# Performance work log

Hardware: AMD Instinct MI355X
Metric: run time of the kernel (lower is better)

## Reference

```python
import jax, jax.numpy as jnp
import numpy as np

DIM = 512
NUM_HEADS = 8
HEAD_DIM = DIM // NUM_HEADS
SCALE = HEAD_DIM ** -0.5


def setup_inputs() -> dict:
    key = jax.random.key(0)
    k1, k2, k3, k4 = jax.random.split(key, 4)
    x = jax.random.normal(k1, (2, 4096, DIM), dtype=jnp.float32)
    # Linear weights stored as (in, out) for x @ W; torch Linear(dim, 3*dim, bias=False)
    w_qkv = jax.random.normal(k2, (DIM, 3 * DIM), dtype=jnp.float32) * (DIM ** -0.5)
    w_proj = jax.random.normal(k3, (DIM, DIM), dtype=jnp.float32) * (DIM ** -0.5)
    b_proj = jax.random.normal(k4, (DIM,), dtype=jnp.float32) * 0.02
    return {"x": x, "w_qkv": w_qkv, "w_proj": w_proj, "b_proj": b_proj}


def reference(x, w_qkv, w_proj, b_proj):
    B, N, C = x.shape
    qkv = (x @ w_qkv).reshape(B, N, 3, NUM_HEADS, HEAD_DIM)
    qkv = jnp.transpose(qkv, (2, 0, 3, 1, 4))  # (3, B, H, N, hd)
    q, k, v = qkv[0], qkv[1], qkv[2]
    attn = jnp.einsum("bhnd,bhmd->bhnm", q, k) * SCALE
    attn = jax.nn.softmax(attn, axis=-1)
    out = jnp.einsum("bhnm,bhmd->bhnd", attn, v)
    out = jnp.transpose(out, (0, 2, 1, 3)).reshape(B, N, C)
    return out @ w_proj + b_proj
```

## Files before the change

kernel.cpp:

```cpp
#include <hip/hip_runtime.h>
#include <hip/hip_bf16.h>
#include <stdint.h>
#include <math.h>

#define NC3 1536
#define QSCALE 0.18033688011111907f
#define KSPLIT 2

typedef __attribute__((ext_vector_type(8))) short short8;
typedef __attribute__((ext_vector_type(4))) short short4v;
typedef __attribute__((ext_vector_type(4))) float f32x4;
typedef __attribute__((ext_vector_type(16))) float f32x16;
typedef __attribute__((ext_vector_type(8))) _Float16 f16x8;
typedef __attribute__((ext_vector_type(2))) __fp16 fp16x2;

static __device__ __forceinline__ short f2bf(float f) {
    union { __hip_bfloat16 h; short s; } u;
    u.h = __float2bfloat16(f);
    return u.s;
}
static __device__ __forceinline__ float bf2f(short s) {
    return __uint_as_float(((unsigned)(unsigned short)s) << 16);
}
static __device__ __forceinline__ short f2h(float f) {
    union { __fp16 h; short s; } u;
    u.h = (__fp16)f;
    return u.s;
}
static __device__ __forceinline__ unsigned hpack(float a, float b) {
    union { fp16x2 h; unsigned u; } c;
    c.h = __builtin_amdgcn_cvt_pkrtz(a, b);
    return c.u;
}

#define GLD_LDS(g, l)                                                          \
    __builtin_amdgcn_global_load_lds(                                          \
        (const __attribute__((address_space(1))) void*)(g),                    \
        (__attribute__((address_space(3))) void*)(l), 16, 0, 0)

__global__ __launch_bounds__(256) void prep(const float* __restrict__ x,
                                            short* __restrict__ xbf,
                                            const float* __restrict__ wqkv,
                                            short* __restrict__ wqkvT,
                                            const float* __restrict__ wproj,
                                            short* __restrict__ wprojT) {
    int tx = threadIdx.x, ty = threadIdx.y;
    int tid = ty * 32 + tx;
    if (blockIdx.z == 0) {
        int bid = blockIdx.y * 48 + blockIdx.x;
        for (int i = bid * 256 + tid; i < 1048576; i += 768 * 256) {
            float4 v = ((const float4*)x)[i];
            short4v o = {f2bf(v.x), f2bf(v.y), f2bf(v.z), f2bf(v.w)};
            ((short4v*)xbf)[i] = o;
        }
        return;
    }
    const float* src;
    short* dst;
    int C;
    bool tof16;
    if (blockIdx.z == 1) { src = wqkv; dst = wqkvT; C = 1536; tof16 = false; }
    else                 { if (blockIdx.x >= 16) return; src = wproj; dst = wprojT; C = 512; tof16 = true; }
    __shared__ short t[32][33];
    int c0 = blockIdx.x * 32, r0 = blockIdx.y * 32;
#pragma unroll
    for (int i = 0; i < 4; i++) {
        float v = src[(size_t)(r0 + ty + i * 8) * C + c0 + tx];
        t[ty + i * 8][tx] = tof16 ? f2h(v) : f2bf(v);
    }
    __syncthreads();
#pragma unroll
    for (int i = 0; i < 4; i++)
        dst[(size_t)(c0 + ty + i * 8) * 512 + r0 + tx] = t[tx][ty + i * 8];
}

__global__ __launch_bounds__(256) void gemm_qkv(const short* __restrict__ A,
                                                const short* __restrict__ Bt,
                                                short* __restrict__ Out,
                                                short* __restrict__ VT) {
    __shared__ __attribute__((aligned(16))) short smem[2][128 * 64];
    short* a_sm = &smem[0][0];
    short* b_sm = &smem[1][0];
    const int tid = threadIdx.x;
    const int lane = tid & 63;
    const int wave = tid >> 6;
    const int wr = wave >> 1, wc = wave & 1;
    const int quad = lane >> 4;
    const int l15 = lane & 15;
    const int m0 = blockIdx.x * 128;
    const int n0 = blockIdx.y * 128;
    const int srow = lane >> 3;
    const int schunk = (lane & 7) ^ srow;

    f32x4 zero4 = {0.f, 0.f, 0.f, 0.f};
    f32x4 acc[4][4];
#pragma unroll
    for (int i = 0; i < 4; i++)
#pragma unroll
        for (int j = 0; j < 4; j++) acc[i][j] = zero4;

    for (int k0 = 0; k0 < 512; k0 += 64) {
        __syncthreads();
#pragma unroll
        for (int i = 0; i < 4; i++) {
            int r0 = wave * 32 + i * 8;
            GLD_LDS(A + (size_t)(m0 + r0 + srow) * 512 + k0 + schunk * 8, a_sm + r0 * 64);
            GLD_LDS(Bt + (size_t)(n0 + r0 + srow) * 512 + k0 + schunk * 8, b_sm + r0 * 64);
        }
        __syncthreads();
#pragma unroll
        for (int kk = 0; kk < 2; kk++) {
            short8 af[4], bfr[4];
#pragma unroll
            for (int mi = 0; mi < 4; mi++) {
                int row = wr * 64 + mi * 16 + l15;
                af[mi] = *(const short8*)(a_sm + row * 64 + (((kk * 4 + quad) ^ (row & 7))) * 8);
            }
#pragma unroll
            for (int ni = 0; ni < 4; ni++) {
                int row = wc * 64 + ni * 16 + l15;
                bfr[ni] = *(const short8*)(b_sm + row * 64 + (((kk * 4 + quad) ^ (row & 7))) * 8);
            }
#pragma unroll
            for (int mi = 0; mi < 4; mi++)
#pragma unroll
                for (int ni = 0; ni < 4; ni++)
                    acc[mi][ni] = __builtin_amdgcn_mfma_f32_16x16x32_bf16(
                        af[mi], bfr[ni], acc[mi][ni], 0, 0, 0);
        }
    }

#pragma unroll
    for (int mi = 0; mi < 4; mi++) {
#pragma unroll
        for (int ni = 0; ni < 4; ni++) {
            int gm0 = m0 + wr * 64 + mi * 16 + quad * 4;
            int gn = n0 + wc * 64 + ni * 16 + l15;
            f32x4 v = acc[mi][ni];
#pragma unroll
            for (int r = 0; r < 4; r++) {
                float val = v[r];
                float o = (gn < 512) ? val * QSCALE : val;
                Out[(size_t)(gm0 + r) * NC3 + gn] = f2bf(o);
            }
        }
    }

    if (n0 >= 1024) {
        __syncthreads();
        short* lt = &smem[0][0];
        const int sq = ((quad & 1) << 1) | (quad >> 1);
#pragma unroll
        for (int mi = 0; mi < 4; mi++) {
#pragma unroll
            for (int ni = 0; ni < 4; ni++) {
                int cl = wc * 64 + ni * 16 + l15;
                int tg = wr * 16 + mi * 4 + sq;
                int tg2 = tg ^ ((cl & 7) << 1);
                f32x4 v = acc[mi][ni];
                uint2 pk;
                pk.x = hpack(v[0], v[1]);
                pk.y = hpack(v[2], v[3]);
                *(uint2*)(lt + cl * 128 + tg2 * 4) = pk;
            }
        }
        __syncthreads();
        int cl = tid >> 1, half = tid & 1;
        int cv = n0 - 1024 + cl;
        int h = cv >> 6, d = cv & 63;
        int btok = m0 >> 12;
        int mt = m0 & 4095;
        short* vrow = VT + ((size_t)((btok * 8 + h) * 64 + d)) * 4096 + mt + half * 64;
        int m = (cl & 7) << 1;
#pragma unroll
        for (int j = 0; j < 8; j++) {
            int tg = half * 16 + j * 2;
            short8 v8 = *(const short8*)(lt + cl * 128 + (tg ^ m) * 4);
            *(short8*)(vrow + j * 8) = v8;
        }
    }
}

__global__ __launch_bounds__(256, 4) void attn_kernel(const short* __restrict__ QKV,
                                                      const short* __restrict__ VT,
                                                      short* __restrict__ Op0,
                                                      short* __restrict__ Op1,
                                                      float* __restrict__ lpart) {
    __shared__ __attribute__((aligned(16))) short k_sm[2][64 * 64];
    __shared__ __attribute__((aligned(16))) short v_sm[2][64 * 64];

    const int tid = threadIdx.x;
    const int lane = tid & 63;
    const int wave = tid >> 6;
    const int l31 = lane & 31;
    const int hi = lane >> 5;
    const int qt = blockIdx.x;
    const int bh = blockIdx.y;
    const int ks = blockIdx.z;
    const int b = bh >> 3, h = bh & 7;
    const size_t tokbase = (size_t)b * 4096;
    const int rowbase = qt * 128;
    const int kt0 = ks * (64 / KSPLIT);
    const int kt1 = kt0 + (64 / KSPLIT);
    const short* Qg = QKV + h * 64;
    const short* Kg = QKV + 512 + h * 64;
    const short* VTg = VT + (size_t)bh * 64 * 4096;
    const int srow = lane >> 3;
    const int schunk = (lane & 7) ^ srow;

    short* qstage = &k_sm[0][0];
#pragma unroll
    for (int i = 0; i < 4; i++) {
        int r0 = wave * 32 + i * 8;
        GLD_LDS(Qg + (tokbase + rowbase + r0 + srow) * NC3 + schunk * 8, qstage + r0 * 64);
    }
    __syncthreads();
    const int qrow = wave * 32 + l31;
    short8 qf[4];
#pragma unroll
    for (int kk = 0; kk < 4; kk++) {
        int slot = (kk * 2 + hi) ^ (qrow & 7);
        qf[kk] = *(const short8*)(qstage + qrow * 64 + slot * 8);
    }
    __syncthreads();

#pragma unroll
    for (int i = 0; i < 2; i++) {
        int r0 = wave * 16 + i * 8;
        GLD_LDS(Kg + (tokbase + (size_t)kt0 * 64 + r0 + srow) * NC3 + schunk * 8,
                k_sm[0] + r0 * 64);
        GLD_LDS(VTg + (size_t)(r0 + srow) * 4096 + kt0 * 64 + schunk * 8,
                v_sm[0] + r0 * 64);
    }

    const _Float16 onef = (_Float16)1.0f;
    const f16x8 ones16 = {onef, onef, onef, onef, onef, onef, onef, onef};

    f32x16 acc_o[2], acc_l;
#pragma unroll
    for (int i = 0; i < 16; i++) { acc_o[0][i] = 0.f; acc_o[1][i] = 0.f; acc_l[i] = 0.f; }

    for (int kt = kt0; kt < kt1; kt++) {
        __syncthreads();
        const int cur = kt & 1;
        if (kt < kt1 - 1) {
            const int nb = cur ^ 1;
#pragma unroll
            for (int i = 0; i < 2; i++) {
                int r0 = wave * 16 + i * 8;
                GLD_LDS(Kg + (tokbase + (size_t)(kt + 1) * 64 + r0 + srow) * NC3 + schunk * 8,
                        k_sm[nb] + r0 * 64);
                GLD_LDS(VTg + (size_t)(r0 + srow) * 4096 + (kt + 1) * 64 + schunk * 8,
                        v_sm[nb] + r0 * 64);
            }
        }

        f32x16 s[2];
#pragma unroll
        for (int i = 0; i < 16; i++) { s[0][i] = 0.f; s[1][i] = 0.f; }
#pragma unroll
        for (int kk = 0; kk < 4; kk++) {
#pragma unroll
            for (int kb = 0; kb < 2; kb++) {
                int row = kb * 32 + l31;
                int slot = (kk * 2 + hi) ^ (row & 7);
                short8 kf = *(const short8*)(k_sm[cur] + row * 64 + slot * 8);
                s[kb] = __builtin_amdgcn_mfma_f32_32x32x16_bf16(kf, qf[kk], s[kb], 0, 0, 0);
            }
        }

        unsigned pk[2][8];
#pragma unroll
        for (int kb = 0; kb < 2; kb++)
#pragma unroll
            for (int i = 0; i < 16; i += 2)
                pk[kb][i >> 1] = hpack(__builtin_amdgcn_exp2f(s[kb][i]),
                                       __builtin_amdgcn_exp2f(s[kb][i + 1]));

#pragma unroll
        for (int g = 0; g < 4; g++) {
            union { unsigned u[4]; f16x8 v; } pf;
#pragma unroll
            for (int t = 0; t < 4; t++) pf.u[t] = pk[g >> 1][4 * (g & 1) + t];
            acc_l = __builtin_amdgcn_mfma_f32_32x32x16_f16(ones16, pf.v, acc_l, 0, 0, 0);
#pragma unroll
            for (int db = 0; db < 2; db++) {
                int row = db * 32 + l31;
                int slot = (g * 2 + hi) ^ (row & 7);
                f16x8 vf = *(const f16x8*)(v_sm[cur] + row * 64 + slot * 8);
                acc_o[db] = __builtin_amdgcn_mfma_f32_32x32x16_f16(vf, pf.v, acc_o[db], 0, 0, 0);
            }
        }
    }

    __syncthreads();

    size_t growq = tokbase + rowbase + qrow;
    if (hi == 0) lpart[(size_t)ks * 65536 + growq * 8 + h] = acc_l[0];

    short* osm = &k_sm[0][0] + wave * 2048;
#pragma unroll
    for (int db = 0; db < 2; db++) {
#pragma unroll
        for (int i = 0; i < 16; i += 2) {
            int d = db * 32 + (i & 3) + 8 * (i >> 2) + 4 * hi;
            unsigned pkd = hpack(acc_o[db][i], acc_o[db][i + 1]);
            int slot = (d >> 3) ^ (l31 & 7);
            *(unsigned*)(osm + l31 * 64 + slot * 8 + (d & 7)) = pkd;
        }
    }
    short* Od = (ks == 0) ? Op0 : Op1;
#pragma unroll
    for (int j = 0; j < 4; j++) {
        int r = lane >> 1;
        int c = (lane & 1) * 4 + j;
        int slot = c ^ (r & 7);
        short8 ov = *(const short8*)(osm + r * 64 + slot * 8);
        size_t grow = tokbase + rowbase + wave * 32 + r;
        *(short8*)(Od + grow * 512 + h * 64 + c * 8) = ov;
    }
}

__global__ __launch_bounds__(256) void gemm_proj(const short* __restrict__ Op0,
                                                 const short* __restrict__ Op1,
                                                 const float* __restrict__ lpart,
                                                 const short* __restrict__ Bt,
                                                 float* __restrict__ OutF,
                                                 const float* __restrict__ bias) {
    __shared__ __attribute__((aligned(16))) short a0_sm[128 * 64];
    __shared__ __attribute__((aligned(16))) short a1_sm[128 * 64];
    __shared__ __attribute__((aligned(16))) short b_sm[64 * 64];
    __shared__ float linv_sm[128 * 8];
    const int tid = threadIdx.x;
    const int lane = tid & 63;
    const int wave = tid >> 6;
    const int wr = wave >> 1, wc = wave & 1;
    const int quad = lane >> 4;
    const int l15 = lane & 15;
    const int m0 = blockIdx.x * 128;
    const int n0 = blockIdx.y * 64;
    const int srow = lane >> 3;
    const int schunk = (lane & 7) ^ srow;

    {
        int idx = tid * 4;
        int row = idx >> 3;
        int hh = idx & 7;
        float4 va = *(const float4*)(lpart + (size_t)(m0 + row) * 8 + hh);
        float4 vb = *(const float4*)(lpart + 65536 + (size_t)(m0 + row) * 8 + hh);
        linv_sm[idx + 0] = 1.0f / (va.x + vb.x);
        linv_sm[idx + 1] = 1.0f / (va.y + vb.y);
        linv_sm[idx + 2] = 1.0f / (va.z + vb.z);
        linv_sm[idx + 3] = 1.0f / (va.w + vb.w);
    }

    f32x4 zero4 = {0.f, 0.f, 0.f, 0.f};
    f32x4 acc[4][2];
#pragma unroll
    for (int i = 0; i < 4; i++) { acc[i][0] = zero4; acc[i][1] = zero4; }

    for (int k0 = 0; k0 < 512; k0 += 64) {
        __syncthreads();
#pragma unroll
        for (int i = 0; i < 4; i++) {
            int r0 = wave * 32 + i * 8;
            GLD_LDS(Op0 + (size_t)(m0 + r0 + srow) * 512 + k0 + schunk * 8, a0_sm + r0 * 64);
            GLD_LDS(Op1 + (size_t)(m0 + r0 + srow) * 512 + k0 + schunk * 8, a1_sm + r0 * 64);
        }
#pragma unroll
        for (int i = 0; i < 2; i++) {
            int r0 = wave * 16 + i * 8;
            GLD_LDS(Bt + (size_t)(n0 + r0 + srow) * 512 + k0 + schunk * 8, b_sm + r0 * 64);
        }
        __syncthreads();
        const int h = k0 >> 6;
#pragma unroll
        for (int kk = 0; kk < 2; kk++) {
            f16x8 af[4], bfr[2];
#pragma unroll
            for (int mi = 0; mi < 4; mi++) {
                int row = wr * 64 + mi * 16 + l15;
                int slot = (kk * 4 + quad) ^ (row & 7);
                f16x8 a0v = *(const f16x8*)(a0_sm + row * 64 + slot * 8);
                f16x8 a1v = *(const f16x8*)(a1_sm + row * 64 + slot * 8);
                _Float16 lh = (_Float16)linv_sm[row * 8 + h];
                f16x8 lv = {lh, lh, lh, lh, lh, lh, lh, lh};
                af[mi] = (a0v + a1v) * lv;
            }
#pragma unroll
            for (int ni = 0; ni < 2; ni++) {
                int row = wc * 32 + ni * 16 + l15;
                int slot = (kk * 4 + quad) ^ (row & 7);
                bfr[ni] = *(const f16x8*)(b_sm + row * 64 + slot * 8);
            }
#pragma unroll
            for (int mi = 0; mi < 4; mi++)
#pragma unroll
                for (int ni = 0; ni < 2; ni++)
                    acc[mi][ni] = __builtin_amdgcn_mfma_f32_16x16x32_f16(
                        af[mi], bfr[ni], acc[mi][ni], 0, 0, 0);
        }
    }

#pragma unroll
    for (int mi = 0; mi < 4; mi++) {
#pragma unroll
        for (int ni = 0; ni < 2; ni++) {
            int gm0 = m0 + wr * 64 + mi * 16 + quad * 4;
            int gn = n0 + wc * 32 + ni * 16 + l15;
            f32x4 v = acc[mi][ni];
#pragma unroll
            for (int r = 0; r < 4; r++)
                OutF[(size_t)(gm0 + r) * 512 + gn] = v[r] + bias[gn];
        }
    }
}

extern "C" void kernel_launch(void* const* d_in, const int* in_sizes, int n_in,
                              void* d_out, int out_size, void* d_ws, size_t ws_size,
                              hipStream_t stream) {
    (void)in_sizes; (void)n_in; (void)out_size; (void)ws_size;
    const float* x = (const float*)d_in[0];
    const float* wqkv = (const float*)d_in[1];
    const float* wproj = (const float*)d_in[2];
    const float* bproj = (const float*)d_in[3];
    float* out = (float*)d_out;

    short* ws = (short*)d_ws;
    short* xbf = ws;
    short* wqkvT = xbf + (size_t)4194304;
    short* wprojT = wqkvT + (size_t)1536 * 512;
    short* QKV = wprojT + (size_t)512 * 512;
    short* VTb = QKV + (size_t)8192 * 1536;
    short* Op0 = VTb + (size_t)16 * 64 * 4096;
    short* Op1 = xbf;
    float* lpart = (float*)wqkvT;

    prep<<<dim3(48, 16, 3), dim3(32, 8), 0, stream>>>(x, xbf, wqkv, wqkvT, wproj, wprojT);
    gemm_qkv<<<dim3(64, 12), 256, 0, stream>>>(xbf, wqkvT, QKV, VTb);
    attn_kernel<<<dim3(32, 16, KSPLIT), 256, 0, stream>>>(QKV, VTb, Op0, Op1, lpart);
    gemm_proj<<<dim3(64, 8), 256, 0, stream>>>(Op0, Op1, lpart, wprojT, out, bproj);
}
```

Measured before the change: 201.5 us.

## Software-pipeline attention QK^T with softmax/PV, remap blocks per XCD

The attention loop is restructured into a two-stage software pipeline. It computes the next tile's QK^T scores while the current tile's exp and PV MFMAs run, prefetches two tiles ahead with a triple-buffered V and explicit vmcnt waits, and raises wave priority during the compute section. The row-sum MFMA against a ones vector is replaced by scalar accumulation plus one cross-half shuffle. Block indices in the QKV GEMM, attention and projection kernels are remapped so blocks sharing data land on the same XCD for better L2 reuse. This adds register pressure from the extra score accumulators and more LDS, which may hurt occupancy under launch_bounds(256,4).

```diff
diff --git a/kernel.cpp b/kernel.cpp
--- a/kernel.cpp
+++ b/kernel.cpp
@@ -37,6 +37,8 @@
     __builtin_amdgcn_global_load_lds(                                          \
         (const __attribute__((address_space(1))) void*)(g),                    \
         (__attribute__((address_space(3))) void*)(l), 16, 0, 0)
+
+#define MEMFENCE asm volatile("" ::: "memory")
 
 __global__ __launch_bounds__(256) void prep(const float* __restrict__ x,
                                             short* __restrict__ xbf,
@@ -87,8 +89,11 @@
     const int wr = wave >> 1, wc = wave & 1;
     const int quad = lane >> 4;
     const int l15 = lane & 15;
-    const int m0 = blockIdx.x * 128;
-    const int n0 = blockIdx.y * 128;
+    const int orig = blockIdx.y * 64 + blockIdx.x;
+    const int xcd = orig & 7;
+    const int lid = orig >> 3;
+    const int m0 = (xcd * 8 + (lid & 7)) * 128;
+    const int n0 = (lid >> 3) * 128;
     const int srow = lane >> 3;
     const int schunk = (lane & 7) ^ srow;
 
@@ -187,21 +192,25 @@
                                                       short* __restrict__ Op1,
                                                       float* __restrict__ lpart) {
     __shared__ __attribute__((aligned(16))) short k_sm[2][64 * 64];
-    __shared__ __attribute__((aligned(16))) short v_sm[2][64 * 64];
+    __shared__ __attribute__((aligned(16))) short v_sm[3][64 * 64];
 
     const int tid = threadIdx.x;
     const int lane = tid & 63;
     const int wave = tid >> 6;
     const int l31 = lane & 31;
     const int hi = lane >> 5;
-    const int qt = blockIdx.x;
-    const int bh = blockIdx.y;
-    const int ks = blockIdx.z;
+    const int orig = (blockIdx.z * 16 + blockIdx.y) * 32 + blockIdx.x;
+    const int xcd = orig & 7;
+    const int lid = orig >> 3;
+    const int qt = lid & 31;
+    const int pr = xcd * 4 + (lid >> 5);
+    const int bh = pr & 15;
+    const int ks = pr >> 4;
     const int b = bh >> 3, h = bh & 7;
     const size_t tokbase = (size_t)b * 4096;
     const int rowbase = qt * 128;
-    const int kt0 = ks * (64 / KSPLIT);
-    const int kt1 = kt0 + (64 / KSPLIT);
+    constexpr int NT = 64 / KSPLIT;
+    const int kt0 = ks * NT;
     const short* Qg = QKV + h * 64;
     const short* Kg = QKV + 512 + h * 64;
     const short* VTg = VT + (size_t)bh * 64 * 4096;
@@ -224,79 +233,138 @@
     }
     __syncthreads();
 
-#pragma unroll
-    for (int i = 0; i < 2; i++) {
-        int r0 = wave * 16 + i * 8;
-        GLD_LDS(Kg + (tokbase + (size_t)kt0 * 64 + r0 + srow) * NC3 + schunk * 8,
-                k_sm[0] + r0 * 64);
-        GLD_LDS(VTg + (size_t)(r0 + srow) * 4096 + kt0 * 64 + schunk * 8,
-                v_sm[0] + r0 * 64);
-    }
-
-    const _Float16 onef = (_Float16)1.0f;
-    const f16x8 ones16 = {onef, onef, onef, onef, onef, onef, onef, onef};
-
-    f32x16 acc_o[2], acc_l;
-#pragma unroll
-    for (int i = 0; i < 16; i++) { acc_o[0][i] = 0.f; acc_o[1][i] = 0.f; acc_l[i] = 0.f; }
-
-    for (int kt = kt0; kt < kt1; kt++) {
-        __syncthreads();
-        const int cur = kt & 1;
-        if (kt < kt1 - 1) {
-            const int nb = cur ^ 1;
-#pragma unroll
-            for (int i = 0; i < 2; i++) {
-                int r0 = wave * 16 + i * 8;
-                GLD_LDS(Kg + (tokbase + (size_t)(kt + 1) * 64 + r0 + srow) * NC3 + schunk * 8,
-                        k_sm[nb] + r0 * 64);
-                GLD_LDS(VTg + (size_t)(r0 + srow) * 4096 + (kt + 1) * 64 + schunk * 8,
-                        v_sm[nb] + r0 * 64);
-            }
-        }
-
-        f32x16 s[2];
-#pragma unroll
-        for (int i = 0; i < 16; i++) { s[0][i] = 0.f; s[1][i] = 0.f; }
-#pragma unroll
-        for (int kk = 0; kk < 4; kk++) {
-#pragma unroll
-            for (int kb = 0; kb < 2; kb++) {
-                int row = kb * 32 + l31;
+    f32x16 acc_o[2];
+#pragma unroll
+    for (int i = 0; i < 16; i++) { acc_o[0][i] = 0.f; acc_o[1][i] = 0.f; }
+    float la0 = 0.f, la1 = 0.f;
+
+    f32x16 sA[2], sB[2];
+
+    int vc = kt0 % 3;
+    {
+        int v1 = vc + 1; if (v1 >= 3) v1 -= 3;
+#pragma unroll
+        for (int j = 0; j < 2; j++) {
+            int r0 = wave * 16 + j * 8;
+            GLD_LDS(Kg + (tokbase + (size_t)kt0 * 64 + r0 + srow) * NC3 + schunk * 8,
+                    &k_sm[0][0] + r0 * 64);
+            GLD_LDS(VTg + (size_t)(r0 + srow) * 4096 + kt0 * 64 + schunk * 8,
+                    &v_sm[vc][0] + r0 * 64);
+        }
+#pragma unroll
+        for (int j = 0; j < 2; j++) {
+            int r0 = wave * 16 + j * 8;
+            GLD_LDS(Kg + (tokbase + (size_t)(kt0 + 1) * 64 + r0 + srow) * NC3 + schunk * 8,
+                    &k_sm[1][0] + r0 * 64);
+            GLD_LDS(VTg + (size_t)(r0 + srow) * 4096 + (kt0 + 1) * 64 + schunk * 8,
+                    &v_sm[v1][0] + r0 * 64);
+        }
+        asm volatile("s_waitcnt vmcnt(4)" ::: "memory");
+        __builtin_amdgcn_s_barrier();
+        MEMFENCE;
+#pragma unroll
+        for (int t = 0; t < 16; t++) { sA[0][t] = 0.f; sA[1][t] = 0.f; }
+#pragma unroll
+        for (int kk = 0; kk < 4; kk++)
+#pragma unroll
+            for (int kbi = 0; kbi < 2; kbi++) {
+                int row = kbi * 32 + l31;
                 int slot = (kk * 2 + hi) ^ (row & 7);
-                short8 kf = *(const short8*)(k_sm[cur] + row * 64 + slot * 8);
-                s[kb] = __builtin_amdgcn_mfma_f32_32x32x16_bf16(kf, qf[kk], s[kb], 0, 0, 0);
-            }
-        }
+                short8 kf = *(const short8*)(&k_sm[0][0] + row * 64 + slot * 8);
+                sA[kbi] = __builtin_amdgcn_mfma_f32_32x32x16_bf16(kf, qf[kk], sA[kbi], 0, 0, 0);
+            }
+        MEMFENCE;
+        __builtin_amdgcn_s_barrier();
+        MEMFENCE;
+    }
+
+    auto body = [&](int i, int p, f32x16 (&Scur)[2], f32x16 (&Snew)[2], int vcur) {
+        const int kt = kt0 + i;
+        if (i + 2 < NT) {
+            int v2 = vcur + 2; if (v2 >= 3) v2 -= 3;
+            short* kdst = &k_sm[p][0];
+            short* vdst = &v_sm[v2][0];
+#pragma unroll
+            for (int j = 0; j < 2; j++) {
+                int r0 = wave * 16 + j * 8;
+                GLD_LDS(Kg + (tokbase + (size_t)(kt + 2) * 64 + r0 + srow) * NC3 + schunk * 8,
+                        kdst + r0 * 64);
+                GLD_LDS(VTg + (size_t)(r0 + srow) * 4096 + (kt + 2) * 64 + schunk * 8,
+                        vdst + r0 * 64);
+            }
+            asm volatile("s_waitcnt vmcnt(4)" ::: "memory");
+        } else {
+            asm volatile("s_waitcnt vmcnt(0)" ::: "memory");
+        }
+        __builtin_amdgcn_s_barrier();
+        MEMFENCE;
+        __builtin_amdgcn_s_setprio(1);
 
         unsigned pk[2][8];
 #pragma unroll
-        for (int kb = 0; kb < 2; kb++)
-#pragma unroll
-            for (int i = 0; i < 16; i += 2)
-                pk[kb][i >> 1] = hpack(__builtin_amdgcn_exp2f(s[kb][i]),
-                                       __builtin_amdgcn_exp2f(s[kb][i + 1]));
-
+        for (int t = 0; t < 16; t += 2) {
+            float e0 = __builtin_amdgcn_exp2f(Scur[0][t]);
+            float e1 = __builtin_amdgcn_exp2f(Scur[0][t + 1]);
+            pk[0][t >> 1] = hpack(e0, e1);
+            la0 += e0 + e1;
+        }
+#pragma unroll
+        for (int t = 0; t < 16; t += 2) {
+            float e0 = __builtin_amdgcn_exp2f(Scur[1][t]);
+            float e1 = __builtin_amdgcn_exp2f(Scur[1][t + 1]);
+            pk[1][t >> 1] = hpack(e0, e1);
+            la1 += e0 + e1;
+        }
+
+        if (i + 1 < NT) {
+#pragma unroll
+            for (int t = 0; t < 16; t++) { Snew[0][t] = 0.f; Snew[1][t] = 0.f; }
+            const short* kbase = &k_sm[p ^ 1][0];
+#pragma unroll
+            for (int kk = 0; kk < 4; kk++)
+#pragma unroll
+                for (int kbi = 0; kbi < 2; kbi++) {
+                    int row = kbi * 32 + l31;
+                    int slot = (kk * 2 + hi) ^ (row & 7);
+                    short8 kf = *(const short8*)(kbase + row * 64 + slot * 8);
+                    Snew[kbi] = __builtin_amdgcn_mfma_f32_32x32x16_bf16(kf, qf[kk], Snew[kbi], 0, 0, 0);
+                }
+        }
+
+        const short* vbase = &v_sm[vcur][0];
 #pragma unroll
         for (int g = 0; g < 4; g++) {
             union { unsigned u[4]; f16x8 v; } pf;
 #pragma unroll
             for (int t = 0; t < 4; t++) pf.u[t] = pk[g >> 1][4 * (g & 1) + t];
-            acc_l = __builtin_amdgcn_mfma_f32_32x32x16_f16(ones16, pf.v, acc_l, 0, 0, 0);
 #pragma unroll
             for (int db = 0; db < 2; db++) {
                 int row = db * 32 + l31;
                 int slot = (g * 2 + hi) ^ (row & 7);
-                f16x8 vf = *(const f16x8*)(v_sm[cur] + row * 64 + slot * 8);
+                f16x8 vf = *(const f16x8*)(vbase + row * 64 + slot * 8);
                 acc_o[db] = __builtin_amdgcn_mfma_f32_32x32x16_f16(vf, pf.v, acc_o[db], 0, 0, 0);
             }
         }
+        __builtin_amdgcn_s_setprio(0);
+        MEMFENCE;
+        __builtin_amdgcn_s_barrier();
+        MEMFENCE;
+    };
+
+#pragma unroll 1
+    for (int i = 0; i < NT; i += 2) {
+        body(i, 0, sA, sB, vc);
+        vc = (vc == 2) ? 0 : vc + 1;
+        body(i + 1, 1, sB, sA, vc);
+        vc = (vc == 2) ? 0 : vc + 1;
     }
 
     __syncthreads();
 
+    float l_acc = la0 + la1;
+    l_acc += __shfl_xor(l_acc, 32);
     size_t growq = tokbase + rowbase + qrow;
-    if (hi == 0) lpart[(size_t)ks * 65536 + growq * 8 + h] = acc_l[0];
+    if (hi == 0) lpart[(size_t)ks * 65536 + growq * 8 + h] = l_acc;
 
     short* osm = &k_sm[0][0] + wave * 2048;
 #pragma unroll
@@ -337,8 +405,11 @@
     const int wr = wave >> 1, wc = wave & 1;
     const int quad = lane >> 4;
     const int l15 = lane & 15;
-    const int m0 = blockIdx.x * 128;
-    const int n0 = blockIdx.y * 64;
+    const int orig = blockIdx.y * 64 + blockIdx.x;
+    const int xcd = orig & 7;
+    const int lid = orig >> 3;
+    const int m0 = (xcd * 8 + (lid & 7)) * 128;
+    const int n0 = (lid >> 3) * 64;
     const int srow = lane >> 3;
     const int schunk = (lane & 7) ^ srow;
 
```

New measurement: 399.1 us. 98.0% more time.
